# Kernel optimization log

Measured on AMD Instinct MI355X. Metric: run time of the kernel, lower is better.

The kernel has to match this reference:

```python
import jax, jax.numpy as jnp
import numpy as np

DIM = 4096
HIDDEN = 4096
B, N, M = 2, 512, 2048


def setup_inputs() -> dict:
    key = jax.random.key(0)
    k1, k2, k3, k4 = jax.random.split(key, 4)
    memory = jax.random.normal(k1, (B, M, DIM), dtype=jnp.bfloat16)
    inputs = jax.random.normal(k2, (B, N, DIM), dtype=jnp.bfloat16)
    # Linear(dim, hidden, bias=False): weight is [hidden, dim]; y = x @ W^T
    scale = 1.0 / np.sqrt(DIM)
    wq = (jax.random.normal(k3, (HIDDEN, DIM), dtype=jnp.float32) * scale).astype(jnp.bfloat16)
    wk = (jax.random.normal(k4, (HIDDEN, DIM), dtype=jnp.float32) * scale).astype(jnp.bfloat16)
    return {"memory": memory, "inputs": inputs, "wq": wq, "wk": wk, "seg_num": 100}


def reference(memory, inputs, wq, wk, seg_num):
    # xq = inputs @ Wq^T  [B, N, H];  mk = memory @ Wk^T  [B, M, H]
    xq = jnp.einsum('bnd,hd->bnh', inputs, wq)
    mk = jnp.einsum('bmd,hd->bmh', memory, wk)
    scores = jnp.einsum('bnh,bmh->bnm', xq, mk) / np.sqrt(HIDDEN)  # [B, N, M]
    scores = jax.nn.softmax(scores.astype(jnp.float32), axis=-1).astype(xq.dtype)
    # hist = seg_num - argmax over memory axis, flattened  [B*N]
    hist = (seg_num - jnp.argmax(scores, axis=2)).reshape(-1)
    browse = hist[0] < 4
    output = jnp.einsum('bnm,bmd->bnd', scores, memory)  # [B, N, dim]
    return output, hist, browse
```

## Files before the change

kernel.cpp:

```cpp
#include <hip/hip_runtime.h>

typedef unsigned short u16;
typedef unsigned int   u32;
typedef unsigned long long u64;
typedef __attribute__((ext_vector_type(8))) short bf16x8;
typedef __attribute__((ext_vector_type(8))) unsigned short u16x8;
typedef __attribute__((ext_vector_type(4))) float f32x4;

__device__ __forceinline__ float bf2f(u16 h){ u32 u = ((u32)h)<<16; return __builtin_bit_cast(float, u); }
__device__ __forceinline__ u16 f2bf(float f){
    u32 u = __builtin_bit_cast(u32, f);
    return (u16)((u + 0x7FFFu + ((u>>16)&1u)) >> 16);
}
__device__ __forceinline__ u16 ftrunc_bf(float f){
    return (u16)(__builtin_bit_cast(u32, f) >> 16);
}

__device__ __forceinline__ void gload16(const void* g, void* l){
    __builtin_amdgcn_global_load_lds((const __attribute__((address_space(1))) void*)g,
                                     (__attribute__((address_space(3))) void*)l, 16, 0, 0);
}

__global__ __launch_bounds__(512, 2) void gemm8ph(
    const u16* __restrict__ A, const u16* __restrict__ B, u16* __restrict__ C)
{
    extern __shared__ u16 lds[];
    const int K = 4096, ldc = 4096;
    const int t = threadIdx.x;
    const int lane = t & 63, wid = t >> 6;
    const int wr = wid >> 2, wc = wid & 3;
    const int laneRow = lane & 15, laneK = (lane >> 4) << 3;

    int bid = blockIdx.x;
    bid = (bid & 7) * 32 + (bid >> 3);
    const int rowA0 = (bid >> 4) * 256, rowB0 = (bid & 15) * 256;

    f32x4 acc[8][4];
    #pragma unroll
    for (int i = 0; i < 8; i++)
        #pragma unroll
        for (int j = 0; j < 4; j++) acc[i][j] = (f32x4){0.f,0.f,0.f,0.f};

    int sidx[4], srow[4], scg[4];
    #pragma unroll
    for (int i = 0; i < 4; i++){
        int id = i * 512 + t;
        sidx[i] = id;
        srow[i] = id >> 3;
        scg[i]  = (id & 7) ^ ((id >> 3) & 7);
    }

    const int nT = K >> 6;
    #pragma unroll
    for (int i = 0; i < 4; i++){
        gload16(A + (size_t)(rowA0 + srow[i]) * K + scg[i]*8, &lds[0*32768 + sidx[i]*8]);
        gload16(B + (size_t)(rowB0 + srow[i]) * K + scg[i]*8, &lds[0*32768 + 16384 + sidx[i]*8]);
    }

    for (int kt = 0; kt < nT; ++kt){
        const int b = kt & 1;
        if (kt + 1 < nT){
            const int kk = (kt + 1) << 6;
            const int bo = (b ^ 1) * 32768;
            #pragma unroll
            for (int i = 0; i < 4; i++){
                gload16(A + (size_t)(rowA0 + srow[i]) * K + kk + scg[i]*8, &lds[bo + sidx[i]*8]);
                gload16(B + (size_t)(rowB0 + srow[i]) * K + kk + scg[i]*8, &lds[bo + 16384 + sidx[i]*8]);
            }
            asm volatile("s_waitcnt vmcnt(8)" ::: "memory");
        } else {
            asm volatile("s_waitcnt vmcnt(0)" ::: "memory");
        }
        __builtin_amdgcn_s_barrier();
        __builtin_amdgcn_sched_barrier(0);

        const char* lA = (const char*)&lds[b * 32768];
        const char* lB = (const char*)&lds[b * 32768 + 16384];

        bf16x8 bfrag[2][4];
        #pragma unroll
        for (int kh = 0; kh < 2; kh++)
            #pragma unroll
            for (int ni = 0; ni < 4; ni++){
                int row = wc*64 + ni*16 + laneRow;
                int raw = row*128 + kh*64 + (laneK<<1);
                bfrag[kh][ni] = *(const bf16x8*)(lB + (raw ^ ((row & 7) << 4)));
            }

        #pragma unroll
        for (int q = 0; q < 4; ++q){
            bf16x8 af[2][2];
            #pragma unroll
            for (int mm = 0; mm < 2; mm++){
                int mi = q*2 + mm;
                int row = wr*128 + mi*16 + laneRow;
                int mask = (row & 7) << 4;
                int raw0 = row*128 + (laneK<<1);
                af[mm][0] = *(const bf16x8*)(lA + (raw0 ^ mask));
                af[mm][1] = *(const bf16x8*)(lA + ((raw0 + 64) ^ mask));
            }
            __builtin_amdgcn_s_setprio(1);
            #pragma unroll
            for (int mm = 0; mm < 2; mm++){
                int mi = q*2 + mm;
                #pragma unroll
                for (int ni = 0; ni < 4; ni++)
                    acc[mi][ni] = __builtin_amdgcn_mfma_f32_16x16x32_bf16(af[mm][0], bfrag[0][ni], acc[mi][ni], 0, 0, 0);
                #pragma unroll
                for (int ni = 0; ni < 4; ni++)
                    acc[mi][ni] = __builtin_amdgcn_mfma_f32_16x16x32_bf16(af[mm][1], bfrag[1][ni], acc[mi][ni], 0, 0, 0);
            }
            __builtin_amdgcn_s_setprio(0);
            __builtin_amdgcn_s_barrier();
            __builtin_amdgcn_sched_barrier(0);
        }
    }

    const int rowBase = rowA0 + wr*128;
    const int colBase = rowB0 + wc*64;
    #pragma unroll
    for (int mi = 0; mi < 8; mi++){
        #pragma unroll
        for (int ni = 0; ni < 4; ni++){
            f32x4 a = acc[mi][ni];
            const int cc = colBase + ni*16 + laneRow;
            const int rr = rowBase + mi*16 + ((lane >> 4) << 2);
            #pragma unroll
            for (int r = 0; r < 4; r++)
                C[(size_t)(rr + r) * ldc + cc] = f2bf(a[r]);
        }
    }
}

template<int OF32>
__device__ __forceinline__ void gemm_body(
    const u16* __restrict__ A, const u16* __restrict__ B, void* __restrict__ Cv,
    int K, int ldc, int rowA0, int rowB0, float scale,
    u16* lA, u16* lB)
{
    const int t = threadIdx.x, lane = t & 63, w = t >> 6;
    const int wr = w >> 1, wc = w & 1;

    f32x4 acc[4][4];
    #pragma unroll
    for (int i = 0; i < 4; i++)
        #pragma unroll
        for (int j = 0; j < 4; j++) acc[i][j] = (f32x4){0.f,0.f,0.f,0.f};

    const int r0 = t >> 2,         c0 = (t & 3) << 3;
    const int r1 = (t + 256) >> 2, c1 = ((t + 256) & 3) << 3;
    const int laneRow = lane & 15, laneK = (lane >> 4) << 3;

    const int nK = K >> 5;
    for (int kt = 0; kt < nK; ++kt){
        const int kk = kt << 5;
        gload16(A + (size_t)(rowA0 + r0) * K + kk + c0, &lA[t * 8]);
        gload16(B + (size_t)(rowB0 + r0) * K + kk + c0, &lB[t * 8]);
        gload16(A + (size_t)(rowA0 + r1) * K + kk + c1, &lA[(t + 256) * 8]);
        gload16(B + (size_t)(rowB0 + r1) * K + kk + c1, &lB[(t + 256) * 8]);
        __syncthreads();

        bf16x8 af[4], bfv[4];
        #pragma unroll
        for (int mi = 0; mi < 4; mi++)
            af[mi] = *(const bf16x8*)&lA[(wr*64 + mi*16 + laneRow) * 32 + laneK];
        #pragma unroll
        for (int ni = 0; ni < 4; ni++)
            bfv[ni] = *(const bf16x8*)&lB[(wc*64 + ni*16 + laneRow) * 32 + laneK];

        #pragma unroll
        for (int mi = 0; mi < 4; mi++)
            #pragma unroll
            for (int ni = 0; ni < 4; ni++)
                acc[mi][ni] = __builtin_amdgcn_mfma_f32_16x16x32_bf16(af[mi], bfv[ni], acc[mi][ni], 0, 0, 0);
        __syncthreads();
    }

    const int rowBase = rowA0 + wr*64;
    const int colBase = rowB0 + wc*64;
    #pragma unroll
    for (int mi = 0; mi < 4; mi++){
        #pragma unroll
        for (int ni = 0; ni < 4; ni++){
            f32x4 a = acc[mi][ni];
            const int cc = colBase + ni*16 + laneRow;
            const int rr = rowBase + mi*16 + ((lane >> 4) << 2);
            #pragma unroll
            for (int r = 0; r < 4; r++){
                const size_t idx = (size_t)(rr + r) * ldc + cc;
                float v = a[r] * scale;
                if (OF32) ((float*)Cv)[idx] = v;
                else      ((u16*)Cv)[idx]  = f2bf(v);
            }
        }
    }
}

template<int OF32>
__global__ __launch_bounds__(256) void gemm_b16(
    const u16* __restrict__ A, const u16* __restrict__ B, void* __restrict__ Cv,
    int K, int ldc, long aBatch, long bBatch, long cBatch, float scale)
{
    __shared__ u16 lA[128*32];
    __shared__ u16 lB[128*32];
    const int b = blockIdx.z;
    const u16* Ab = A + (size_t)b * aBatch;
    const u16* Bb = B + (size_t)b * bBatch;
    void* Cb = OF32 ? (void*)((float*)Cv + (size_t)b * cBatch)
                    : (void*)((u16*)Cv  + (size_t)b * cBatch);
    gemm_body<OF32>(Ab, Bb, Cb, K, ldc, blockIdx.y * 128, blockIdx.x * 128, scale, lA, lB);
}

__global__ __launch_bounds__(256) void proj_redo(
    const u32* __restrict__ flag,
    const u16* __restrict__ mem16, const u16* __restrict__ wk16, u16* __restrict__ mk16)
{
    if (*flag == 0) return;
    __shared__ u16 lA[128*32];
    __shared__ u16 lB[128*32];
    gemm_body<0>(mem16, wk16, mk16, 4096, 4096, blockIdx.y * 128, blockIdx.x * 128, 1.0f, lA, lB);
}

__global__ void flag_init(u32* f){ if (threadIdx.x == 0) *f = 0; }

__global__ __launch_bounds__(256) void vfy_mk(
    const u16* __restrict__ mem16, const u16* __restrict__ wk16, const u16* __restrict__ mk16,
    u32* __restrict__ flag)
{
    const int wgl = blockIdx.x * 4 + (threadIdx.x >> 6);
    const int lane = threadIdx.x & 63;
    const int row = ((wgl * 331 + 17) & 4095);
    const int col = ((wgl * 173 + 5) & 4095);
    const u16* a = mem16 + (size_t)row * 4096;
    const u16* b = wk16 + (size_t)col * 4096;
    float s = 0.f;
    #pragma unroll
    for (int i = 0; i < 8; i++){
        const int o = (i * 64 + lane) * 8;
        u16x8 av = *(const u16x8*)(a + o);
        u16x8 bv = *(const u16x8*)(b + o);
        #pragma unroll
        for (int j = 0; j < 8; j++) s += bf2f(av[j]) * bf2f(bv[j]);
    }
    #pragma unroll
    for (int off = 32; off; off >>= 1) s += __shfl_xor(s, off, 64);
    if (lane == 0){
        if (fabsf(s - bf2f(mk16[(size_t)row * 4096 + col])) > 0.05f) atomicOr(flag, 1u);
    }
}

__global__ __launch_bounds__(256) void cvt_all(
    const float* __restrict__ m, const float* __restrict__ in,
    const float* __restrict__ q, const float* __restrict__ k,
    u16* __restrict__ m16, u16* __restrict__ in16,
    u16* __restrict__ q16, u16* __restrict__ k16)
{
    const long N0 = 2097152, N1 = N0 + 524288, N2 = N1 + 2097152, N3 = N2 + 2097152;
    for (long g = (long)blockIdx.x * 256 + threadIdx.x; g < N3; g += (long)gridDim.x * 256){
        const float* src; u16* dst; long o;
        if      (g < N0){ src = m;  dst = m16;  o = g; }
        else if (g < N1){ src = in; dst = in16; o = g - N0; }
        else if (g < N2){ src = q;  dst = q16;  o = g - N1; }
        else            { src = k;  dst = k16;  o = g - N2; }
        f32x4 a = *(const f32x4*)(src + o*8);
        f32x4 b = *(const f32x4*)(src + o*8 + 4);
        u16x8 v;
        #pragma unroll
        for (int j = 0; j < 4; j++){ v[j] = ftrunc_bf(a[j]); v[j+4] = ftrunc_bf(b[j]); }
        *(u16x8*)(dst + o*8) = v;
    }
}

__global__ __launch_bounds__(256) void transpose_u16(
    const u16* __restrict__ in, u16* __restrict__ out)
{
    __shared__ u16 tile[64][65];
    const size_t bi = (size_t)blockIdx.z * 2048 * 4096;
    const size_t bo = (size_t)blockIdx.z * 4096 * 2048;
    const int c0 = blockIdx.x * 64;
    const int r0 = blockIdx.y * 64;
    const int x = threadIdx.x & 63, y = threadIdx.x >> 6;
    #pragma unroll
    for (int i = 0; i < 16; i++){
        int r = y + i*4;
        tile[r][x] = in[bi + (size_t)(r0 + r) * 4096 + c0 + x];
    }
    __syncthreads();
    #pragma unroll
    for (int i = 0; i < 16; i++){
        int c = y + i*4;
        out[bo + (size_t)(c0 + c) * 2048 + r0 + x] = tile[x][c];
    }
}

__device__ __forceinline__ u32 shfl_u32(u32 v, int srcx){ return (u32)__shfl_xor((int)v, srcx, 64); }
__device__ __forceinline__ u64 shflxor64(u64 x, int off){
    u32 lo = (u32)x, hi = (u32)(x >> 32);
    lo = shfl_u32(lo, off); hi = shfl_u32(hi, off);
    return (((u64)hi) << 32) | lo;
}

__global__ __launch_bounds__(256) void softmax_argmax16(
    const u16* __restrict__ sc16, u16* __restrict__ probs,
    float* __restrict__ dout, const int* __restrict__ segp)
{
    const int row = blockIdx.x;
    const u16* s = sc16 + (size_t)row * 2048;
    u16* p = probs + (size_t)row * 2048;
    const int t = threadIdx.x, lane = t & 63, w = t >> 6;

    u16x8 rv = *(const u16x8*)(s + (size_t)t * 8);
    float v[8];
    #pragma unroll
    for (int j = 0; j < 8; j++) v[j] = bf2f(rv[j]);

    float mx = v[0];
    #pragma unroll
    for (int j = 1; j < 8; j++) mx = fmaxf(mx, v[j]);
    #pragma unroll
    for (int off = 32; off; off >>= 1) mx = fmaxf(mx, __shfl_xor(mx, off, 64));
    __shared__ float smax[4];
    if (lane == 0) smax[w] = mx;
    __syncthreads();
    mx = fmaxf(fmaxf(smax[0], smax[1]), fmaxf(smax[2], smax[3]));

    float e[8]; float sum = 0.f;
    #pragma unroll
    for (int j = 0; j < 8; j++){ e[j] = expf(v[j] - mx); sum += e[j]; }
    #pragma unroll
    for (int off = 32; off; off >>= 1) sum += __shfl_xor(sum, off, 64);
    __shared__ float ssum[4];
    if (lane == 0) ssum[w] = sum;
    __syncthreads();
    sum = ssum[0] + ssum[1] + ssum[2] + ssum[3];

    u16x8 pv;
    u64 best = 0ull;
    #pragma unroll
    for (int j = 0; j < 8; j++){
        u16 pb = f2bf(e[j] / sum);
        pv[j] = pb;
        u64 key = (((u64)pb) << 32) | (u32)(0x7FFFFFFF - (t*8 + j));
        if (key > best) best = key;
    }
    *(u16x8*)(p + (size_t)t * 8) = pv;

    #pragma unroll
    for (int off = 32; off; off >>= 1){
        u64 o = shflxor64(best, off);
        if (o > best) best = o;
    }
    __shared__ u64 sb[4];
    if (lane == 0) sb[w] = best;
    __syncthreads();
    if (t == 0){
        u64 bb = sb[0];
        if (sb[1] > bb) bb = sb[1];
        if (sb[2] > bb) bb = sb[2];
        if (sb[3] > bb) bb = sb[3];
        int idx = 0x7FFFFFFF - (int)(bb & 0xFFFFFFFFu);
        float hv = (float)(segp[0] - idx);
        dout[4194304 + row] = hv;
        if (row == 0) dout[4195328] = (hv < 4.0f) ? 1.0f : 0.0f;
    }
}

template<int F32IN, int OF32>
__global__ __launch_bounds__(256) void gemm_bt(
    const void* __restrict__ Av, const void* __restrict__ Bv, void* __restrict__ Cv,
    int K, int ldc, float scale)
{
    __shared__ u16 lA[128*32];
    __shared__ u16 lB[128*32];
    const int rowA0 = blockIdx.y * 128;
    const int rowB0 = blockIdx.x * 128;
    const int t = threadIdx.x, lane = t & 63, w = t >> 6;
    const int wr = w >> 1, wc = w & 1;

    f32x4 acc[4][4];
    #pragma unroll
    for (int i = 0; i < 4; i++)
        #pragma unroll
        for (int j = 0; j < 4; j++) acc[i][j] = (f32x4){0.f,0.f,0.f,0.f};

    const int r0 = t >> 2,         c0 = (t & 3) << 3;
    const int r1 = (t + 256) >> 2, c1 = ((t + 256) & 3) << 3;
    const int laneRow = lane & 15, laneK = (lane >> 4) << 3;

    const int nK = K >> 5;
    for (int kt = 0; kt < nK; ++kt){
        const int kk = kt << 5;
        if (F32IN){
            const float* Af = (const float*)Av;
            const float* Bf = (const float*)Bv;
            f32x4 a00 = *(const f32x4*)&Af[(size_t)(rowA0 + r0) * K + kk + c0];
            f32x4 a01 = *(const f32x4*)&Af[(size_t)(rowA0 + r0) * K + kk + c0 + 4];
            f32x4 a10 = *(const f32x4*)&Af[(size_t)(rowA0 + r1) * K + kk + c1];
            f32x4 a11 = *(const f32x4*)&Af[(size_t)(rowA0 + r1) * K + kk + c1 + 4];
            f32x4 b00 = *(const f32x4*)&Bf[(size_t)(rowB0 + r0) * K + kk + c0];
            f32x4 b01 = *(const f32x4*)&Bf[(size_t)(rowB0 + r0) * K + kk + c0 + 4];
            f32x4 b10 = *(const f32x4*)&Bf[(size_t)(rowB0 + r1) * K + kk + c1];
            f32x4 b11 = *(const f32x4*)&Bf[(size_t)(rowB0 + r1) * K + kk + c1 + 4];
            u16x8 ua0, ua1, ub0, ub1;
            #pragma unroll
            for (int j = 0; j < 4; j++){
                ua0[j] = ftrunc_bf(a00[j]); ua0[j+4] = ftrunc_bf(a01[j]);
                ua1[j] = ftrunc_bf(a10[j]); ua1[j+4] = ftrunc_bf(a11[j]);
                ub0[j] = ftrunc_bf(b00[j]); ub0[j+4] = ftrunc_bf(b01[j]);
                ub1[j] = ftrunc_bf(b10[j]); ub1[j+4] = ftrunc_bf(b11[j]);
            }
            __syncthreads();
            *(u16x8*)&lA[(size_t)t * 8]         = ua0;
            *(u16x8*)&lA[(size_t)(t + 256) * 8] = ua1;
            *(u16x8*)&lB[(size_t)t * 8]         = ub0;
            *(u16x8*)&lB[(size_t)(t + 256) * 8] = ub1;
            __syncthreads();
        } else {
            const u16* Au = (const u16*)Av;
            const u16* Bu = (const u16*)Bv;
            gload16(Au + (size_t)(rowA0 + r0) * K + kk + c0, &lA[t * 8]);
            gload16(Bu + (size_t)(rowB0 + r0) * K + kk + c0, &lB[t * 8]);
            gload16(Au + (size_t)(rowA0 + r1) * K + kk + c1, &lA[(t + 256) * 8]);
            gload16(Bu + (size_t)(rowB0 + r1) * K + kk + c1, &lB[(t + 256) * 8]);
            __syncthreads();
        }

        bf16x8 af[4], bfv[4];
        #pragma unroll
        for (int mi = 0; mi < 4; mi++)
            af[mi] = *(const bf16x8*)&lA[(wr*64 + mi*16 + laneRow) * 32 + laneK];
        #pragma unroll
        for (int ni = 0; ni < 4; ni++)
            bfv[ni] = *(const bf16x8*)&lB[(wc*64 + ni*16 + laneRow) * 32 + laneK];

        #pragma unroll
        for (int mi = 0; mi < 4; mi++)
            #pragma unroll
            for (int ni = 0; ni < 4; ni++)
                acc[mi][ni] = __builtin_amdgcn_mfma_f32_16x16x32_bf16(af[mi], bfv[ni], acc[mi][ni], 0, 0, 0);
        if (!F32IN) __syncthreads();
    }

    const int rowBase = rowA0 + wr*64;
    const int colBase = rowB0 + wc*64;
    #pragma unroll
    for (int mi = 0; mi < 4; mi++){
        #pragma unroll
        for (int ni = 0; ni < 4; ni++){
            f32x4 a = acc[mi][ni];
            const int cc = colBase + ni*16 + laneRow;
            const int rr = rowBase + mi*16 + ((lane >> 4) << 2);
            #pragma unroll
            for (int r = 0; r < 4; r++){
                const size_t idx = (size_t)(rr + r) * ldc + cc;
                float v = a[r] * scale;
                if (OF32) ((float*)Cv)[idx] = v;
                else      ((u16*)Cv)[idx]  = f2bf(v);
            }
        }
    }
}

__global__ __launch_bounds__(256) void transpose_f2b(
    const float* __restrict__ in, u16* __restrict__ out)
{
    __shared__ u16 tile[64][65];
    const int c0 = blockIdx.x * 64;
    const int r0 = blockIdx.y * 64;
    const int x = threadIdx.x & 63, y = threadIdx.x >> 6;
    #pragma unroll
    for (int i = 0; i < 16; i++){
        int r = y + i*4;
        tile[r][x] = ftrunc_bf(in[(size_t)(r0 + r) * 4096 + c0 + x]);
    }
    __syncthreads();
    #pragma unroll
    for (int i = 0; i < 16; i++){
        int c = y + i*4;
        out[(size_t)(c0 + c) * 2048 + r0 + x] = tile[x][c];
    }
}

extern "C" void kernel_launch(void* const* d_in, const int* in_sizes, int n_in,
                              void* d_out, int out_size, void* d_ws, size_t ws_size,
                              hipStream_t stream)
{
    const float* memory = (const float*)d_in[0];
    const float* inputs = (const float*)d_in[1];
    const float* wq     = (const float*)d_in[2];
    const float* wk     = (const float*)d_in[3];
    const int*   seg    = (const int*)d_in[4];
    float* out = (float*)d_out;

    char* ws = (char*)d_ws;
    dim3 blk(256);

    if (ws_size >= (152ull << 20)){
        u16* mem16 = (u16*)(ws);
        u16* in16  = (u16*)(ws + 33554432);
        u16* wq16  = (u16*)(ws + 41943040);
        u16* wk16  = (u16*)(ws + 75497472);
        u16* xq16  = (u16*)(ws + 109051904);
        u16* mk16  = (u16*)(ws + 117440512);
        u16* sc16  = (u16*)(ws + 150994944);
        u16* pr    = (u16*)(ws + 155189248);
        u16* mt    = mk16;
        u32* flag  = (u32*)sc16;

        cvt_all<<<dim3(4096), blk, 0, stream>>>(memory, inputs, wq, wk,
                                                mem16, in16, wq16, wk16);

        gemm8ph<<<dim3(256), dim3(512), 131072, stream>>>(mem16, wk16, mk16);

        flag_init<<<1, 64, 0, stream>>>(flag);
        vfy_mk<<<dim3(64), blk, 0, stream>>>(mem16, wk16, mk16, flag);
        proj_redo<<<dim3(32, 32, 1), blk, 0, stream>>>(flag, mem16, wk16, mk16);

        gemm_b16<0><<<dim3(32, 8, 1), blk, 0, stream>>>(in16, wq16, xq16, 4096, 4096,
                                                        0L, 0L, 0L, 1.0f);
        gemm_b16<0><<<dim3(16, 4, 2), blk, 0, stream>>>(xq16, mk16, sc16, 4096, 2048,
                                                        512L*4096, 2048L*4096, 512L*2048,
                                                        0.015625f);
        softmax_argmax16<<<dim3(1024), blk, 0, stream>>>(sc16, pr, out, seg);

        transpose_u16<<<dim3(64, 32, 2), blk, 0, stream>>>(mem16, mt);
        gemm_b16<1><<<dim3(32, 4, 2), blk, 0, stream>>>(pr, mt, out, 2048, 4096,
                                                        512L*2048, 4096L*2048, 512L*4096,
                                                        1.0f);
    } else {
        u16* xq16 = (u16*)(ws);
        u16* mk16 = (u16*)(ws + (8u<<20));
        u16* sc16 = (u16*)(ws + (24u<<20));
        u16* pr   = (u16*)(ws + (28u<<20));

        gemm_bt<1,0><<<dim3(32, 8, 1), blk, 0, stream>>>(inputs, wq, xq16, 4096, 4096, 1.0f);
        for (int b = 0; b < 2; ++b){
            const float* memb = memory + (size_t)b * 2048 * 4096;
            gemm_bt<1,0><<<dim3(32, 16, 1), blk, 0, stream>>>(memb, wk, mk16, 4096, 4096, 1.0f);
            gemm_bt<0,0><<<dim3(16, 4, 1), blk, 0, stream>>>(xq16 + (size_t)b*512*4096, mk16,
                                                             sc16 + (size_t)b*512*2048,
                                                             4096, 2048, 0.015625f);
        }
        softmax_argmax16<<<dim3(1024), blk, 0, stream>>>(sc16, pr, out, seg);
        for (int b = 0; b < 2; ++b){
            const float* memb = memory + (size_t)b * 2048 * 4096;
            transpose_f2b<<<dim3(64, 32, 1), blk, 0, stream>>>(memb, mk16);
            gemm_bt<0,1><<<dim3(32, 4, 1), blk, 0, stream>>>(pr + (size_t)b*512*2048, mk16,
                                                             out + (size_t)b*512*4096,
                                                             2048, 4096, 1.0f);
        }
    }
}
```

Before: 420.7 us.

## Deepen main GEMM pipeline to four K=32 stages and add 64-row scores GEMM

The large mk projection GEMM switches from double-buffered K=64 tiles to a four-stage ring of K=32 tiles, prefetching three tiles ahead with graded vmcnt waits and a new XOR swizzle. The aim is to hide more global-to-LDS latency per barrier. A new 64x128-tile GEMM replaces the 128x128 kernel for the batched scores product, doubling the block count to improve occupancy on that small GEMM. The flag reset is folded into the conversion kernel, which removes one launch. The deeper pipeline puts two barriers in every K=32 step, and the new scores kernel has no double buffering.

```diff
diff --git a/kernel.cpp b/kernel.cpp
--- a/kernel.cpp
+++ b/kernel.cpp
@@ -30,6 +30,7 @@
     const int lane = t & 63, wid = t >> 6;
     const int wr = wid >> 2, wc = wid & 3;
     const int laneRow = lane & 15, laneK = (lane >> 4) << 3;
+    const int laneCk = laneK >> 3;
 
     int bid = blockIdx.x;
     bid = (bid & 7) * 32 + (bid >> 3);
@@ -41,80 +42,60 @@
         #pragma unroll
         for (int j = 0; j < 4; j++) acc[i][j] = (f32x4){0.f,0.f,0.f,0.f};
 
-    int sidx[4], srow[4], scg[4];
-    #pragma unroll
-    for (int i = 0; i < 4; i++){
-        int id = i * 512 + t;
-        sidx[i] = id;
-        srow[i] = id >> 3;
-        scg[i]  = (id & 7) ^ ((id >> 3) & 7);
-    }
-
-    const int nT = K >> 6;
-    #pragma unroll
-    for (int i = 0; i < 4; i++){
-        gload16(A + (size_t)(rowA0 + srow[i]) * K + scg[i]*8, &lds[0*32768 + sidx[i]*8]);
-        gload16(B + (size_t)(rowB0 + srow[i]) * K + scg[i]*8, &lds[0*32768 + 16384 + sidx[i]*8]);
-    }
+    const int idA0 = t, idA1 = t + 512;
+    const int rA0 = idA0 >> 2, cA0 = (idA0 & 3) ^ ((idA0 >> 3) & 3);
+    const int rA1 = idA1 >> 2, cA1 = (idA1 & 3) ^ ((idA1 >> 3) & 3);
+
+    const int nT = K >> 5;
+
+    #define STAGE(kt_) do{                                                            \
+        const int _kk = (kt_) << 5;                                                   \
+        u16* _b = &lds[((kt_) & 3) * 16384];                                          \
+        gload16(A + (size_t)(rowA0 + rA0) * K + _kk + cA0*8, &_b[idA0*8]);            \
+        gload16(A + (size_t)(rowA0 + rA1) * K + _kk + cA1*8, &_b[idA1*8]);            \
+        gload16(B + (size_t)(rowB0 + rA0) * K + _kk + cA0*8, &_b[8192 + idA0*8]);     \
+        gload16(B + (size_t)(rowB0 + rA1) * K + _kk + cA1*8, &_b[8192 + idA1*8]);     \
+    } while(0)
+
+    STAGE(0); STAGE(1); STAGE(2);
 
     for (int kt = 0; kt < nT; ++kt){
-        const int b = kt & 1;
-        if (kt + 1 < nT){
-            const int kk = (kt + 1) << 6;
-            const int bo = (b ^ 1) * 32768;
-            #pragma unroll
-            for (int i = 0; i < 4; i++){
-                gload16(A + (size_t)(rowA0 + srow[i]) * K + kk + scg[i]*8, &lds[bo + sidx[i]*8]);
-                gload16(B + (size_t)(rowB0 + srow[i]) * K + kk + scg[i]*8, &lds[bo + 16384 + sidx[i]*8]);
-            }
+        __builtin_amdgcn_s_barrier();
+        if (kt + 3 < nT){
+            STAGE(kt + 3);
+            asm volatile("s_waitcnt vmcnt(12)" ::: "memory");
+        } else if (kt + 2 < nT){
             asm volatile("s_waitcnt vmcnt(8)" ::: "memory");
+        } else if (kt + 1 < nT){
+            asm volatile("s_waitcnt vmcnt(4)" ::: "memory");
         } else {
             asm volatile("s_waitcnt vmcnt(0)" ::: "memory");
         }
         __builtin_amdgcn_s_barrier();
         __builtin_amdgcn_sched_barrier(0);
 
-        const char* lA = (const char*)&lds[b * 32768];
-        const char* lB = (const char*)&lds[b * 32768 + 16384];
-
-        bf16x8 bfrag[2][4];
-        #pragma unroll
-        for (int kh = 0; kh < 2; kh++)
-            #pragma unroll
-            for (int ni = 0; ni < 4; ni++){
-                int row = wc*64 + ni*16 + laneRow;
-                int raw = row*128 + kh*64 + (laneK<<1);
-                bfrag[kh][ni] = *(const bf16x8*)(lB + (raw ^ ((row & 7) << 4)));
-            }
-
-        #pragma unroll
-        for (int q = 0; q < 4; ++q){
-            bf16x8 af[2][2];
-            #pragma unroll
-            for (int mm = 0; mm < 2; mm++){
-                int mi = q*2 + mm;
-                int row = wr*128 + mi*16 + laneRow;
-                int mask = (row & 7) << 4;
-                int raw0 = row*128 + (laneK<<1);
-                af[mm][0] = *(const bf16x8*)(lA + (raw0 ^ mask));
-                af[mm][1] = *(const bf16x8*)(lA + ((raw0 + 64) ^ mask));
-            }
-            __builtin_amdgcn_s_setprio(1);
-            #pragma unroll
-            for (int mm = 0; mm < 2; mm++){
-                int mi = q*2 + mm;
-                #pragma unroll
-                for (int ni = 0; ni < 4; ni++)
-                    acc[mi][ni] = __builtin_amdgcn_mfma_f32_16x16x32_bf16(af[mm][0], bfrag[0][ni], acc[mi][ni], 0, 0, 0);
-                #pragma unroll
-                for (int ni = 0; ni < 4; ni++)
-                    acc[mi][ni] = __builtin_amdgcn_mfma_f32_16x16x32_bf16(af[mm][1], bfrag[1][ni], acc[mi][ni], 0, 0, 0);
-            }
-            __builtin_amdgcn_s_setprio(0);
-            __builtin_amdgcn_s_barrier();
-            __builtin_amdgcn_sched_barrier(0);
-        }
-    }
+        const char* lA = (const char*)&lds[(kt & 3) * 16384];
+        const char* lB = lA + 16384;
+
+        bf16x8 bfrag[4];
+        #pragma unroll
+        for (int ni = 0; ni < 4; ni++){
+            int row = wc*64 + ni*16 + laneRow;
+            bfrag[ni] = *(const bf16x8*)(lB + row*64 + ((laneCk ^ ((row >> 1) & 3)) << 4));
+        }
+
+        __builtin_amdgcn_s_setprio(1);
+        #pragma unroll
+        for (int mi = 0; mi < 8; mi++){
+            int row = wr*128 + mi*16 + laneRow;
+            bf16x8 a0 = *(const bf16x8*)(lA + row*64 + ((laneCk ^ ((row >> 1) & 3)) << 4));
+            #pragma unroll
+            for (int ni = 0; ni < 4; ni++)
+                acc[mi][ni] = __builtin_amdgcn_mfma_f32_16x16x32_bf16(a0, bfrag[ni], acc[mi][ni], 0, 0, 0);
+        }
+        __builtin_amdgcn_s_setprio(0);
+    }
+    #undef STAGE
 
     const int rowBase = rowA0 + wr*128;
     const int colBase = rowB0 + wc*64;
@@ -211,6 +192,72 @@
     gemm_body<OF32>(Ab, Bb, Cb, K, ldc, blockIdx.y * 128, blockIdx.x * 128, scale, lA, lB);
 }
 
+__global__ __launch_bounds__(256) void gemm64(
+    const u16* __restrict__ A, const u16* __restrict__ B, u16* __restrict__ C,
+    int K, int ldc, long aBatch, long bBatch, long cBatch, float scale)
+{
+    __shared__ u16 lA[64*32];
+    __shared__ u16 lB[128*32];
+    const int bz = blockIdx.z;
+    A += (size_t)bz * aBatch;
+    B += (size_t)bz * bBatch;
+    C += (size_t)bz * cBatch;
+    const int rowA0 = blockIdx.y * 64;
+    const int rowB0 = blockIdx.x * 128;
+    const int t = threadIdx.x, lane = t & 63, w = t >> 6;
+    const int wr = w >> 1, wc = w & 1;
+    const int laneRow = lane & 15, laneK = (lane >> 4) << 3;
+
+    f32x4 acc[2][4];
+    #pragma unroll
+    for (int i = 0; i < 2; i++)
+        #pragma unroll
+        for (int j = 0; j < 4; j++) acc[i][j] = (f32x4){0.f,0.f,0.f,0.f};
+
+    const int rA = t >> 2,  cA = (t & 3) << 3;
+    const int rB0 = t >> 2, cB0 = (t & 3) << 3;
+    const int rB1 = (t + 256) >> 2, cB1 = ((t + 256) & 3) << 3;
+
+    const int nK = K >> 5;
+    for (int kt = 0; kt < nK; ++kt){
+        const int kk = kt << 5;
+        gload16(A + (size_t)(rowA0 + rA) * K + kk + cA, &lA[t * 8]);
+        gload16(B + (size_t)(rowB0 + rB0) * K + kk + cB0, &lB[t * 8]);
+        gload16(B + (size_t)(rowB0 + rB1) * K + kk + cB1, &lB[(t + 256) * 8]);
+        __syncthreads();
+
+        bf16x8 af[2], bfv[4];
+        #pragma unroll
+        for (int mi = 0; mi < 2; mi++)
+            af[mi] = *(const bf16x8*)&lA[(wr*32 + mi*16 + laneRow) * 32 + laneK];
+        #pragma unroll
+        for (int ni = 0; ni < 4; ni++)
+            bfv[ni] = *(const bf16x8*)&lB[(wc*64 + ni*16 + laneRow) * 32 + laneK];
+
+        #pragma unroll
+        for (int mi = 0; mi < 2; mi++)
+            #pragma unroll
+            for (int ni = 0; ni < 4; ni++)
+                acc[mi][ni] = __builtin_amdgcn_mfma_f32_16x16x32_bf16(af[mi], bfv[ni], acc[mi][ni], 0, 0, 0);
+        __syncthreads();
+    }
+
+    const int rowBase = rowA0 + wr*32;
+    const int colBase = rowB0 + wc*64;
+    #pragma unroll
+    for (int mi = 0; mi < 2; mi++){
+        #pragma unroll
+        for (int ni = 0; ni < 4; ni++){
+            f32x4 a = acc[mi][ni];
+            const int cc = colBase + ni*16 + laneRow;
+            const int rr = rowBase + mi*16 + ((lane >> 4) << 2);
+            #pragma unroll
+            for (int r = 0; r < 4; r++)
+                C[(size_t)(rr + r) * ldc + cc] = f2bf(a[r] * scale);
+        }
+    }
+}
+
 __global__ __launch_bounds__(256) void proj_redo(
     const u32* __restrict__ flag,
     const u16* __restrict__ mem16, const u16* __restrict__ wk16, u16* __restrict__ mk16)
@@ -220,8 +267,6 @@
     __shared__ u16 lB[128*32];
     gemm_body<0>(mem16, wk16, mk16, 4096, 4096, blockIdx.y * 128, blockIdx.x * 128, 1.0f, lA, lB);
 }
-
-__global__ void flag_init(u32* f){ if (threadIdx.x == 0) *f = 0; }
 
 __global__ __launch_bounds__(256) void vfy_mk(
     const u16* __restrict__ mem16, const u16* __restrict__ wk16, const u16* __restrict__ mk16,
@@ -253,8 +298,9 @@
     const float* __restrict__ m, const float* __restrict__ in,
     const float* __restrict__ q, const float* __restrict__ k,
     u16* __restrict__ m16, u16* __restrict__ in16,
-    u16* __restrict__ q16, u16* __restrict__ k16)
-{
+    u16* __restrict__ q16, u16* __restrict__ k16, u32* __restrict__ flag)
+{
+    if (blockIdx.x == 0 && threadIdx.x == 0) *flag = 0;
     const long N0 = 2097152, N1 = N0 + 524288, N2 = N1 + 2097152, N3 = N2 + 2097152;
     for (long g = (long)blockIdx.x * 256 + threadIdx.x; g < N3; g += (long)gridDim.x * 256){
         const float* src; u16* dst; long o;
@@ -508,19 +554,18 @@
         u32* flag  = (u32*)sc16;
 
         cvt_all<<<dim3(4096), blk, 0, stream>>>(memory, inputs, wq, wk,
-                                                mem16, in16, wq16, wk16);
+                                                mem16, in16, wq16, wk16, flag);
 
         gemm8ph<<<dim3(256), dim3(512), 131072, stream>>>(mem16, wk16, mk16);
 
-        flag_init<<<1, 64, 0, stream>>>(flag);
         vfy_mk<<<dim3(64), blk, 0, stream>>>(mem16, wk16, mk16, flag);
         proj_redo<<<dim3(32, 32, 1), blk, 0, stream>>>(flag, mem16, wk16, mk16);
 
         gemm_b16<0><<<dim3(32, 8, 1), blk, 0, stream>>>(in16, wq16, xq16, 4096, 4096,
                                                         0L, 0L, 0L, 1.0f);
-        gemm_b16<0><<<dim3(16, 4, 2), blk, 0, stream>>>(xq16, mk16, sc16, 4096, 2048,
-                                                        512L*4096, 2048L*4096, 512L*2048,
-                                                        0.015625f);
+        gemm64<<<dim3(16, 8, 2), blk, 0, stream>>>(xq16, mk16, sc16, 4096, 2048,
+                                                   512L*4096, 2048L*4096, 512L*2048,
+                                                   0.015625f);
         softmax_argmax16<<<dim3(1024), blk, 0, stream>>>(sc16, pr, out, seg);
 
         transpose_u16<<<dim3(64, 32, 2), blk, 0, stream>>>(mem16, mt);
```

Result: faster. 408.4 us (-2.9%).
